# Kernel tuning notes

Measured on AMD Instinct MI355X. Metric: run time of the kernel, lower is better.

Reference implementation:

```python
import jax, jax.numpy as jnp
import numpy as np

N_NODES = 50000
N_EDGES = 500000
NUM_FEAT = 128
NUM_CLASSES = 112
HID = 18
HEADS = 8
OUT_DIM = 144  # hidden_dim * heads = 18*8 = 144, also final GAT out_dim
N_GRAPHS = 64
EPS = 1e-5
NEG_SLOPE = 0.2


def setup_inputs() -> dict:
    key = jax.random.key(0)
    ks = jax.random.split(key, 32)
    f32 = jnp.float32
    def rn(k, shape, scale=0.1):
        return jax.random.normal(k, shape, f32) * scale
    x = jax.random.normal(ks[0], (N_NODES, NUM_FEAT), f32)
    edge_index = jax.random.randint(ks[1], (2, N_EDGES), 0, N_NODES)
    batch = jnp.sort(jax.random.randint(ks[2], (N_NODES,), 0, N_GRAPHS))
    D = HID * HEADS  # 144
    params = dict(
        x=x, edge_index=edge_index, batch=batch,
        We=rn(ks[3], (NUM_FEAT, D)), be=jnp.zeros((D,), f32),
        Wg=rn(ks[4], (3, D, D)),
        a_sg=rn(ks[5], (3, HEADS, HID)), a_dg=rn(ks[6], (3, HEADS, HID)),
        bg=jnp.zeros((3, D), f32),
        gam=jnp.ones((3, D), f32), bet=jnp.zeros((3, D), f32),
        W3=rn(ks[7], (D, OUT_DIM)),
        a_s3=rn(ks[8], (1, OUT_DIM)), a_d3=rn(ks[9], (1, OUT_DIM)),
        b3=jnp.zeros((OUT_DIM,), f32),
        gam3=jnp.ones((OUT_DIM,), f32), bet3=jnp.zeros((OUT_DIM,), f32),
        M1=rn(ks[10], (OUT_DIM, 72)), bm1=jnp.zeros((72,), f32),
        gm1=jnp.ones((72,), f32), bb1=jnp.zeros((72,), f32),
        M2=rn(ks[11], (72, 36)), bm2=jnp.zeros((36,), f32),
        gm2=jnp.ones((36,), f32), bb2=jnp.zeros((36,), f32),
        M3=rn(ks[12], (36, NUM_CLASSES)), bm3=jnp.zeros((NUM_CLASSES,), f32),
    )
    return params


def _gat_layer(h, src, dst, W, a_s, a_d, b, heads, out_ch):
    # PyG GATConv: per-head linear, additive attention, segment softmax over dst
    N = h.shape[0]
    hp = (h @ W).reshape(N, heads, out_ch)                 # [N,H,C]
    al_s = (hp * a_s).sum(-1)                              # [N,H]
    al_d = (hp * a_d).sum(-1)                              # [N,H]
    e = jax.nn.leaky_relu(al_s[src] + al_d[dst], NEG_SLOPE)  # [E,H]
    m = jax.ops.segment_max(e, dst, num_segments=N)
    ex = jnp.exp(e - m[dst])
    den = jax.ops.segment_sum(ex, dst, num_segments=N)
    alpha = ex / (den[dst] + 1e-16)                        # [E,H]
    out = jax.ops.segment_sum(hp[src] * alpha[..., None], dst, num_segments=N)
    return out.reshape(N, heads * out_ch) + b


def _bn(x, g, b):
    mu = x.mean(0)
    v = jnp.var(x, axis=0)
    return g * (x - mu) * jax.lax.rsqrt(v + EPS) + b


def reference(x, edge_index, batch, We, be, Wg, a_sg, a_dg, bg, gam, bet,
              W3, a_s3, a_d3, b3, gam3, bet3,
              M1, bm1, gm1, bb1, M2, bm2, gm2, bb2, M3, bm3):
    N = x.shape[0]
    loops = jnp.arange(N)  # GATConv add_self_loops=True
    src = jnp.concatenate([edge_index[0], loops])
    dst = jnp.concatenate([edge_index[1], loops])
    out = x @ We + be
    for i in range(3):
        out = _gat_layer(out, src, dst, Wg[i], a_sg[i], a_dg[i], bg[i], HEADS, HID)
        out = jax.nn.relu(out)
        out = _bn(out, gam[i], bet[i])
    out = _gat_layer(out, src, dst, W3, a_s3, a_d3, b3, 1, OUT_DIM)
    out = jax.nn.relu(out)
    out = _bn(out, gam3, bet3)
    # global mean pool over graphs
    sums = jax.ops.segment_sum(out, batch, num_segments=N_GRAPHS)
    cnt = jax.ops.segment_sum(jnp.ones((N, 1), out.dtype), batch, num_segments=N_GRAPHS)
    g = sums / jnp.maximum(cnt, 1.0)
    # PyG MLP: lin -> batchnorm -> relu (plain last layer)
    h = jax.nn.relu(_bn(g @ M1 + bm1, gm1, bb1))
    h = jax.nn.relu(_bn(h @ M2 + bm2, gm2, bb2))
    return h @ M3 + bm3
```

## Files before the change

kernel.cpp:

```cpp
#include <hip/hip_runtime.h>
#include <cstdint>

#define N_NODESC 50000
#define N_EDGESC 500000
#define E_TOT    550000
#define DIM      144
#define NGRAPH   64
#define EPSV     1e-5f
#define SCAN_NB  ((N_NODESC + 511)/512)

typedef __attribute__((ext_vector_type(8))) short bf16x8;
typedef __attribute__((ext_vector_type(4))) float f32x4;

__device__ __forceinline__ float lrelu(float x){ return x > 0.f ? x : 0.2f*x; }

__device__ __forceinline__ unsigned short f2bf(float f){
  unsigned u = __float_as_uint(f);
  u += 0x7FFF + ((u >> 16) & 1);
  return (unsigned short)(u >> 16);
}
__device__ __forceinline__ float bf2f(unsigned short b){
  return __uint_as_float(((unsigned)b) << 16);
}

__global__ void k_count(const int* __restrict__ ei, int* __restrict__ deg){
  int e = blockIdx.x*blockDim.x + threadIdx.x;
  if (e >= E_TOT) return;
  int d = (e < N_EDGESC) ? ei[N_EDGESC + e] : (e - N_EDGESC);
  atomicAdd(&deg[d], 1);
}

__global__ __launch_bounds__(256) void k_scan1(const int* __restrict__ deg,
    int* __restrict__ scanned, int* __restrict__ bsum){
  __shared__ int ls[256];
  int b = blockIdx.x, t = threadIdx.x;
  int i0 = b*512 + 2*t;
  int e0 = (i0   < N_NODESC) ? deg[i0]   : 0;
  int e1 = (i0+1 < N_NODESC) ? deg[i0+1] : 0;
  int s = e0 + e1;
  ls[t] = s;
  __syncthreads();
  #pragma unroll
  for (int ofs=1; ofs<256; ofs<<=1){
    int v = (t >= ofs) ? ls[t-ofs] : 0;
    __syncthreads();
    ls[t] += v;
    __syncthreads();
  }
  int excl = ls[t] - s;
  if (i0   < N_NODESC) scanned[i0]   = excl;
  if (i0+1 < N_NODESC) scanned[i0+1] = excl + e0;
  if (t == 255) bsum[b] = ls[255];
}

__global__ void k_scan2(int* __restrict__ bsum){
  __shared__ int ls[128];
  int t = threadIdx.x;
  int v = (t < SCAN_NB) ? bsum[t] : 0;
  ls[t] = v;
  __syncthreads();
  #pragma unroll
  for (int ofs=1; ofs<128; ofs<<=1){
    int u = (t >= ofs) ? ls[t-ofs] : 0;
    __syncthreads();
    ls[t] += u;
    __syncthreads();
  }
  if (t < SCAN_NB) bsum[t] = ls[t] - v;
}

__global__ __launch_bounds__(256) void k_scan3(const int* __restrict__ scanned,
    const int* __restrict__ bsum, int* __restrict__ row_ptr, int* __restrict__ cursor){
  int i = blockIdx.x*blockDim.x + threadIdx.x;
  if (i < N_NODESC){
    int v = scanned[i] + bsum[i >> 9];
    row_ptr[i] = v; cursor[i] = v;
  }
  if (i == 0) row_ptr[N_NODESC] = E_TOT;
}

__global__ void k_scatter(const int* __restrict__ ei, int* __restrict__ cursor,
                          int* __restrict__ col){
  int e = blockIdx.x*blockDim.x + threadIdx.x;
  if (e >= E_TOT) return;
  int s, d;
  if (e < N_EDGESC){ s = ei[e]; d = ei[N_EDGESC + e]; } else { s = e - N_EDGESC; d = s; }
  int pos = atomicAdd(&cursor[d], 1);
  col[pos] = s;
}

__global__ __launch_bounds__(192) void k_prep_w(
    const float* __restrict__ W, const float* __restrict__ bias_in,
    const float* __restrict__ a_s, const float* __restrict__ a_d,
    const float* __restrict__ bnsum, const float* __restrict__ bngam,
    const float* __restrict__ bnbet,
    unsigned short* __restrict__ Wt, float* __restrict__ bias2,
    int K, int SK, int H){
  __shared__ float red[256];
  int np = blockIdx.x, k = threadIdx.x;
  float sc = 1.f, sh = 0.f;
  if (k < K && bnsum){
    float mu  = bnsum[k] * (1.f/N_NODESC);
    float var = bnsum[K+k] * (1.f/N_NODESC) - mu*mu;
    float inv = rsqrtf(var + EPSV);
    sc = inv * bngam[k];
    sh = bnbet[k] - mu*sc;
  }
  float wcomb = 0.f;
  if (k < K){
    if (np < 144) wcomb = W[(size_t)k*144 + np];
    else if (H > 0){
      int c = np - 144;
      bool iss = c < 8;
      int h = iss ? c : c - 8;
      if (h < H){
        const float* av = iss ? a_s : a_d;
        int C = 144 / H;
        for (int j=0;j<C;++j) wcomb += W[(size_t)k*144 + h*C + j] * av[h*C + j];
      }
    }
  }
  if (k < SK) Wt[(size_t)np*SK + k] = f2bf(wcomb*sc);
  red[k] = (k < K) ? sh*wcomb : 0.f;
  if (k < 64) red[k+192] = 0.f;
  __syncthreads();
  #pragma unroll
  for (int s=128; s>0; s>>=1){
    if (k < s) red[k] += red[k+s];
    __syncthreads();
  }
  if (k == 0){
    float b = red[0];
    if (np < 144 && bias_in) b += bias_in[np];
    bias2[np] = b;
  }
}

template<int NT, int KS, int SK, int NROW, int AF32>
__global__ __launch_bounds__(256) void k_mfma_gemm(
    const void* __restrict__ Av,
    const unsigned short* __restrict__ Wt,
    const float* __restrict__ bias2,
    unsigned short* __restrict__ hp,
    float* __restrict__ al_s, float* __restrict__ al_d,
    int KA, int H){
  __shared__ unsigned short sW[NROW*SK];
  int t = threadIdx.x;
  for (int i = t; i < NROW*SK/8; i += 256)
    ((uint4*)sW)[i] = ((const uint4*)Wt)[i];
  __syncthreads();

  int wave = t >> 6, lane = t & 63;
  int c = lane & 15, quad = lane >> 4;
  int m_base = blockIdx.x*64 + wave*16;
  int mA = m_base + c; if (mA > N_NODESC-1) mA = N_NODESC-1;
  f32x4 acc[NT];
  #pragma unroll
  for (int i=0;i<NT;++i) acc[i] = (f32x4){0.f,0.f,0.f,0.f};
  #pragma unroll
  for (int ks=0; ks<KS; ++ks){
    bf16x8 af;
    if (AF32){
      const float* Arow = (const float*)Av + (size_t)mA*KA + quad*8;
      float4 f0 = *(const float4*)(Arow + ks*32);
      float4 f1 = *(const float4*)(Arow + ks*32 + 4);
      unsigned short tmp[8] = { f2bf(f0.x),f2bf(f0.y),f2bf(f0.z),f2bf(f0.w),
                                f2bf(f1.x),f2bf(f1.y),f2bf(f1.z),f2bf(f1.w) };
      af = *(const bf16x8*)tmp;
    } else {
      const unsigned short* Arow = (const unsigned short*)Av + (size_t)mA*KA + quad*8;
      af = *(const bf16x8*)(Arow + ks*32);
    }
    #pragma unroll
    for (int tt=0; tt<NT; ++tt){
      bf16x8 bfr = *(const bf16x8*)(sW + (tt*16 + c)*SK + ks*32 + quad*8);
      acc[tt] = __builtin_amdgcn_mfma_f32_16x16x32_bf16(af, bfr, acc[tt], 0, 0, 0);
    }
  }
  #pragma unroll
  for (int tt=0; tt<NT; ++tt){
    int n = tt*16 + c;
    float b = bias2[n];
    #pragma unroll
    for (int r=0;r<4;++r){
      int m = m_base + quad*4 + r;
      if (m < N_NODESC){
        float v = acc[tt][r] + b;
        if (n < 144){
          hp[(size_t)m*144 + n] = f2bf(v);
        } else {
          int cc = n - 144;
          if (cc < 8){ if (cc < H) al_s[m*H + cc] = v; }
          else { int h = cc - 8; if (h < H) al_d[m*H + h] = v; }
        }
      }
    }
  }
}

#define EB 8
__global__ __launch_bounds__(256) void k_edge_softmax(
    const float* __restrict__ al_s, const float* __restrict__ al_d,
    const int* __restrict__ row_ptr, const int* __restrict__ col,
    float* __restrict__ esc, int H){
  int idx = blockIdx.x*blockDim.x + threadIdx.x;
  if (idx >= N_NODESC*H) return;
  int n = idx / H, h = idx - n*H;
  int p0 = row_ptr[n], p1 = row_ptr[n+1];
  float ald = al_d[idx];
  float m = -3.4e38f, d = 0.f;
  for (int base = p0; base < p1; base += EB){
    int cnt = min(EB, p1 - base);
    int ss[EB];
    #pragma unroll
    for (int i=0;i<EB;++i) if (i<cnt) ss[i] = col[base+i];
    float sc[EB];
    #pragma unroll
    for (int i=0;i<EB;++i) if (i<cnt) sc[i] = lrelu(al_s[ss[i]*H + h] + ald);
    float bm = -3.4e38f;
    #pragma unroll
    for (int i=0;i<EB;++i) if (i<cnt){
      esc[(size_t)(base+i)*H + h] = sc[i];
      bm = fmaxf(bm, sc[i]);
    }
    if (bm > m){ d *= __expf(m - bm); m = bm; }
    #pragma unroll
    for (int i=0;i<EB;++i) if (i<cnt) d += __expf(sc[i] - m);
  }
  float inv = 1.f/(d + 1e-16f);
  for (int e = p0; e < p1; ++e)
    esc[(size_t)e*H + h] = __expf(esc[(size_t)e*H + h] - m) * inv;
}

__global__ __launch_bounds__(256) void k_aggregate2(
    const unsigned* __restrict__ hp2, const float* __restrict__ w,
    const int* __restrict__ row_ptr, const int* __restrict__ col,
    const float* __restrict__ bias, unsigned* __restrict__ out,
    int H, int C2){
  int idx = blockIdx.x*blockDim.x + threadIdx.x;
  if (idx >= N_NODESC*72) return;
  int n = idx / 72, cp = idx - n*72;
  int h = cp / C2;
  int p0 = row_ptr[n], p1 = row_ptr[n+1];
  float a0 = 0.f, a1 = 0.f;
  for (int base = p0; base < p1; base += EB){
    int cnt = min(EB, p1 - base);
    int ss[EB]; float ww[EB];
    #pragma unroll
    for (int i=0;i<EB;++i) if (i<cnt){
      ss[i] = col[base+i];
      ww[i] = w[(size_t)(base+i)*H + h];
    }
    unsigned vv[EB];
    #pragma unroll
    for (int i=0;i<EB;++i) if (i<cnt) vv[i] = hp2[(size_t)ss[i]*72 + cp];
    #pragma unroll
    for (int i=0;i<EB;++i) if (i<cnt){
      a0 = fmaf(ww[i], __uint_as_float(vv[i] << 16), a0);
      a1 = fmaf(ww[i], __uint_as_float(vv[i] & 0xFFFF0000u), a1);
    }
  }
  int c0 = 2*cp;
  float r0 = fmaxf(a0 + bias[c0],   0.f);
  float r1 = fmaxf(a1 + bias[c0+1], 0.f);
  out[(size_t)n*72 + cp] = (unsigned)f2bf(r0) | ((unsigned)f2bf(r1) << 16);
}

#define BNS_GRID 512
__global__ __launch_bounds__(256) void k_bnstats1(const uint2* __restrict__ h4,
                                                  float* __restrict__ partials){
  __shared__ float red[252*8];
  int t = threadIdx.x;
  int r = t / 36, c = t - r*36;
  bool active = (t < 252);
  int rows = (N_NODESC + BNS_GRID - 1)/BNS_GRID;
  int n0 = blockIdx.x*rows, n1 = min(N_NODESC, n0+rows);
  float s[4] = {0,0,0,0}, q[4] = {0,0,0,0};
  if (active){
    for (int n = n0 + r; n < n1; n += 7){
      uint2 v = h4[(size_t)n*36 + c];
      float f0 = __uint_as_float(v.x << 16);
      float f1 = __uint_as_float(v.x & 0xFFFF0000u);
      float f2 = __uint_as_float(v.y << 16);
      float f3 = __uint_as_float(v.y & 0xFFFF0000u);
      s[0]+=f0; q[0]+=f0*f0; s[1]+=f1; q[1]+=f1*f1;
      s[2]+=f2; q[2]+=f2*f2; s[3]+=f3; q[3]+=f3*f3;
    }
    #pragma unroll
    for (int j=0;j<4;++j){
      red[(c*7+r)*8 + j]     = s[j];
      red[(c*7+r)*8 + 4 + j] = q[j];
    }
  }
  __syncthreads();
  if (t < 36){
    float ss[4]={0,0,0,0}, qq[4]={0,0,0,0};
    for (int rr=0; rr<7; ++rr){
      #pragma unroll
      for (int j=0;j<4;++j){
        ss[j] += red[(t*7+rr)*8 + j];
        qq[j] += red[(t*7+rr)*8 + 4 + j];
      }
    }
    float* p = partials + (size_t)blockIdx.x*288;
    #pragma unroll
    for (int j=0;j<4;++j){
      p[4*t+j]       = ss[j];
      p[144+4*t+j]   = qq[j];
    }
  }
}

__global__ __launch_bounds__(64) void k_bnstats2(const float* __restrict__ partials,
                                                 float* __restrict__ sums){
  int i = blockIdx.x, t = threadIdx.x;
  float s = 0.f;
  for (int b = t; b < BNS_GRID; b += 64) s += partials[(size_t)b*288 + i];
  #pragma unroll
  for (int o=32; o>0; o>>=1) s += __shfl_xor(s, o, 64);
  if (t == 0) sums[i] = s;
}

__device__ int lbound(const int* a, int n, int v){
  int lo = 0, hi = n;
  while (lo < hi){ int m = (lo+hi) >> 1; if (a[m] < v) lo = m+1; else hi = m; }
  return lo;
}

__global__ __launch_bounds__(128) void k_pool(const unsigned* __restrict__ h2,
    const int* __restrict__ batch, float* __restrict__ sums, int* __restrict__ cnts){
  int g = blockIdx.x & 63, part = blockIdx.x >> 6;
  __shared__ int sb[2];
  if (threadIdx.x == 0){ sb[0] = lbound(batch, N_NODESC, g); sb[1] = lbound(batch, N_NODESC, g+1); }
  __syncthreads();
  int lo = sb[0], hi = sb[1];
  int t = threadIdx.x;
  if (t < 72){
    float a0 = 0.f, a1 = 0.f;
    for (int n = lo + part; n < hi; n += 32){
      unsigned v = h2[(size_t)n*72 + t];
      a0 += __uint_as_float(v << 16);
      a1 += __uint_as_float(v & 0xFFFF0000u);
    }
    atomicAdd(&sums[g*DIM + 2*t],   a0);
    atomicAdd(&sums[g*DIM + 2*t+1], a1);
  }
  if (t == 0 && part == 0) cnts[g] = hi - lo;
}

__global__ __launch_bounds__(64) void k_mlp1(const float* __restrict__ psum,
    const int* __restrict__ cnts,
    const float* __restrict__ bn3, const float* __restrict__ gam3,
    const float* __restrict__ bet3,
    const float* __restrict__ M1, const float* __restrict__ bm1,
    const float* __restrict__ gm1, const float* __restrict__ bb1,
    float* __restrict__ h1){
  __shared__ float sSc[144], sSh[144];
  int t = threadIdx.x, c = blockIdx.x;
  for (int i=t; i<144; i+=64){
    float mu  = bn3[i] * (1.f/N_NODESC);
    float var = bn3[144+i] * (1.f/N_NODESC) - mu*mu;
    float sc  = rsqrtf(var + EPSV) * gam3[i];
    sSc[i] = sc; sSh[i] = bet3[i] - mu*sc;
  }
  __syncthreads();
  float invc = 1.f / (float)max(cnts[t], 1);
  float acc = bm1[c];
  const float* pr = psum + t*144;
  for (int k=0; k<144; ++k){
    float g = fmaf(pr[k]*invc, sSc[k], sSh[k]);
    acc = fmaf(g, M1[k*72 + c], acc);
  }
  float s = acc, q = acc*acc;
  #pragma unroll
  for (int o=32; o>0; o>>=1){ s += __shfl_xor(s, o, 64); q += __shfl_xor(q, o, 64); }
  float mu = s*(1.f/64.f), var = q*(1.f/64.f) - mu*mu;
  float v = (acc - mu)*rsqrtf(var + EPSV)*gm1[c] + bb1[c];
  h1[t*72 + c] = fmaxf(v, 0.f);
}

__global__ __launch_bounds__(64) void k_mlp2(const float* __restrict__ h1,
    const float* __restrict__ M2, const float* __restrict__ bm2,
    const float* __restrict__ gm2, const float* __restrict__ bb2,
    float* __restrict__ h2){
  int t = threadIdx.x, c = blockIdx.x;
  float acc = bm2[c];
  const float* pr = h1 + t*72;
  for (int k=0; k<72; ++k) acc = fmaf(pr[k], M2[k*36 + c], acc);
  float s = acc, q = acc*acc;
  #pragma unroll
  for (int o=32; o>0; o>>=1){ s += __shfl_xor(s, o, 64); q += __shfl_xor(q, o, 64); }
  float mu = s*(1.f/64.f), var = q*(1.f/64.f) - mu*mu;
  float v = (acc - mu)*rsqrtf(var + EPSV)*gm2[c] + bb2[c];
  h2[t*36 + c] = fmaxf(v, 0.f);
}

__global__ __launch_bounds__(64) void k_mlp3(const float* __restrict__ h2,
    const float* __restrict__ M3, const float* __restrict__ bm3,
    float* __restrict__ out){
  int t = threadIdx.x, c = blockIdx.x;
  float acc = bm3[c];
  const float* pr = h2 + t*36;
  for (int k=0; k<36; ++k) acc = fmaf(pr[k], M3[k*112 + c], acc);
  out[t*112 + c] = acc;
}

extern "C" void kernel_launch(void* const* d_in, const int* in_sizes, int n_in,
                              void* d_out, int out_size, void* d_ws, size_t ws_size,
                              hipStream_t stream){
  const float* x    = (const float*)d_in[0];
  const int*   ei   = (const int*)d_in[1];
  const int*   batch= (const int*)d_in[2];
  const float* We   = (const float*)d_in[3];
  const float* be   = (const float*)d_in[4];
  const float* Wg   = (const float*)d_in[5];
  const float* a_sg = (const float*)d_in[6];
  const float* a_dg = (const float*)d_in[7];
  const float* bg   = (const float*)d_in[8];
  const float* gam  = (const float*)d_in[9];
  const float* bet  = (const float*)d_in[10];
  const float* W3   = (const float*)d_in[11];
  const float* a_s3 = (const float*)d_in[12];
  const float* a_d3 = (const float*)d_in[13];
  const float* b3   = (const float*)d_in[14];
  const float* gam3 = (const float*)d_in[15];
  const float* bet3 = (const float*)d_in[16];
  const float* M1   = (const float*)d_in[17];
  const float* bm1  = (const float*)d_in[18];
  const float* gm1  = (const float*)d_in[19];
  const float* bb1  = (const float*)d_in[20];
  const float* M2   = (const float*)d_in[21];
  const float* bm2  = (const float*)d_in[22];
  const float* gm2  = (const float*)d_in[23];
  const float* bb2  = (const float*)d_in[24];
  const float* M3   = (const float*)d_in[25];
  const float* bm3  = (const float*)d_in[26];
  float* out = (float*)d_out;

  char* ws = (char*)d_ws;
  size_t off = 0;
  auto alloc = [&](size_t bytes)->char*{
    char* p = ws + off; off += (bytes + 255) & ~(size_t)255; return p;
  };
  unsigned short* hAb = (unsigned short*)alloc((size_t)N_NODESC*DIM*2);
  unsigned short* hp  = (unsigned short*)alloc((size_t)N_NODESC*DIM*2);
  float* al_s   = (float*)alloc((size_t)N_NODESC*8*4);
  float* al_d   = (float*)alloc((size_t)N_NODESC*8*4);
  float* esc    = (float*)alloc((size_t)E_TOT*8*4);
  int* row_ptr  = (int*)alloc((size_t)(N_NODESC+1)*4);
  int* deg      = (int*)alloc((size_t)N_NODESC*4);
  int* cursor   = (int*)alloc((size_t)N_NODESC*4);
  int* scanned  = (int*)alloc((size_t)N_NODESC*4);
  int* bsum     = (int*)alloc((size_t)SCAN_NB*4);
  int* col      = (int*)alloc((size_t)E_TOT*4);
  float* bns4   = (float*)alloc(4*2*DIM*4);
  float* partials = (float*)alloc((size_t)BNS_GRID*288*4);
  float* psum   = (float*)alloc((size_t)NGRAPH*DIM*4);
  int* pcnt     = (int*)alloc(NGRAPH*4);
  float* h1buf  = (float*)alloc((size_t)NGRAPH*72*4);
  float* h2buf  = (float*)alloc((size_t)NGRAPH*36*4);
  unsigned short* Wt = (unsigned short*)alloc((size_t)160*168*2);
  float* bias2  = (float*)alloc(160*4);
  (void)ws_size; (void)n_in; (void)in_sizes; (void)out_size;

  const int GEMM_GRID = (N_NODESC + 63)/64;

  hipMemsetAsync(deg, 0, (size_t)N_NODESC*4, stream);
  k_count<<<(E_TOT+255)/256, 256, 0, stream>>>(ei, deg);
  k_scan1<<<SCAN_NB, 256, 0, stream>>>(deg, scanned, bsum);
  k_scan2<<<1, 128, 0, stream>>>(bsum);
  k_scan3<<<(N_NODESC+255)/256, 256, 0, stream>>>(scanned, bsum, row_ptr, cursor);
  k_scatter<<<(E_TOT+255)/256, 256, 0, stream>>>(ei, cursor, col);

  k_prep_w<<<144, 192, 0, stream>>>(We, be, nullptr, nullptr,
                                    nullptr, nullptr, nullptr, Wt, bias2, 128, 136, 0);
  k_mfma_gemm<9,4,136,144,1><<<GEMM_GRID, 256, 0, stream>>>(
      x, Wt, bias2, hAb, nullptr, nullptr, 128, 0);

  for (int L=0; L<4; ++L){
    const float* W  = (L<3) ? (Wg  + (size_t)L*DIM*DIM) : W3;
    const float* as = (L<3) ? (a_sg + (size_t)L*8*18)   : a_s3;
    const float* ad = (L<3) ? (a_dg + (size_t)L*8*18)   : a_d3;
    const float* bb = (L<3) ? (bg  + L*DIM) : b3;
    int H = (L<3) ? 8 : 1;
    int C = (L<3) ? 18 : 144;
    const float* bnp = (L==0) ? nullptr : bns4 + (size_t)(L-1)*2*DIM;
    const float* gmp = (L==0) ? nullptr : gam + (size_t)(L-1)*DIM;
    const float* btp = (L==0) ? nullptr : bet + (size_t)(L-1)*DIM;
    k_prep_w<<<160, 192, 0, stream>>>(W, nullptr, as, ad,
                                      bnp, gmp, btp, Wt, bias2, 144, 168, H);
    k_mfma_gemm<10,5,168,160,0><<<GEMM_GRID, 256, 0, stream>>>(
        hAb, Wt, bias2, hp, al_s, al_d, 144, H);
    k_edge_softmax<<<(N_NODESC*H+255)/256, 256, 0, stream>>>(
        al_s, al_d, row_ptr, col, esc, H);
    k_aggregate2<<<(N_NODESC*72+255)/256, 256, 0, stream>>>(
        (const unsigned*)hp, esc, row_ptr, col, bb, (unsigned*)hAb, H, C/2);
    k_bnstats1<<<BNS_GRID, 256, 0, stream>>>((const uint2*)hAb, partials);
    k_bnstats2<<<288, 64, 0, stream>>>(partials, bns4 + (size_t)L*2*DIM);
  }

  hipMemsetAsync(psum, 0, (size_t)NGRAPH*DIM*4, stream);
  k_pool<<<NGRAPH*32, 128, 0, stream>>>((const unsigned*)hAb, batch, psum, pcnt);
  k_mlp1<<<72, 64, 0, stream>>>(psum, pcnt, bns4 + 3*2*DIM, gam3, bet3,
                                M1, bm1, gm1, bb1, h1buf);
  k_mlp2<<<36, 64, 0, stream>>>(h1buf, M2, bm2, gm2, bb2, h2buf);
  k_mlp3<<<112, 64, 0, stream>>>(h2buf, M3, bm3, out);
}
```

Baseline: 643.6 us.

## Stage GEMM output through LDS for coalesced stores; recompute edge scores instead of storing

The projection GEMM epilogue now writes the bf16 hp tile into shared memory and then copies full 144-wide rows to global memory with 16-byte stores, replacing scattered 2-byte writes. The attention logits are still written directly. The edge softmax kernel no longer writes raw scores in its first pass and rereads them later. It recomputes the scores from al_s gathers in a second pass, trading one global write and read per edge for extra gathers and leaky-relu work. The staging reuses the sW weight buffer behind syncthreads and assumes 64 rows per block.

```diff
diff --git a/kernel.cpp b/kernel.cpp
--- a/kernel.cpp
+++ b/kernel.cpp
@@ -177,24 +177,38 @@
       acc[tt] = __builtin_amdgcn_mfma_f32_16x16x32_bf16(af, bfr, acc[tt], 0, 0, 0);
     }
   }
-  #pragma unroll
-  for (int tt=0; tt<NT; ++tt){
-    int n = tt*16 + c;
+
+  if (NT > 9){
+    int n = 144 + c;
     float b = bias2[n];
     #pragma unroll
     for (int r=0;r<4;++r){
       int m = m_base + quad*4 + r;
       if (m < N_NODESC){
-        float v = acc[tt][r] + b;
-        if (n < 144){
-          hp[(size_t)m*144 + n] = f2bf(v);
-        } else {
-          int cc = n - 144;
-          if (cc < 8){ if (cc < H) al_s[m*H + cc] = v; }
-          else { int h = cc - 8; if (h < H) al_d[m*H + h] = v; }
-        }
+        float v = acc[9][r] + b;
+        if (c < 8){ if (c < H) al_s[m*H + c] = v; }
+        else { int h = c - 8; if (h < H) al_d[m*H + h] = v; }
       }
     }
+  }
+
+  __syncthreads();
+  unsigned short* sOut = sW + wave*2304;
+  #pragma unroll
+  for (int tt=0; tt<9; ++tt){
+    int n = tt*16 + c;
+    float b = bias2[n];
+    #pragma unroll
+    for (int r=0;r<4;++r)
+      sOut[(quad*4+r)*144 + n] = f2bf(acc[tt][r] + b);
+  }
+  __syncthreads();
+  int base_row = blockIdx.x*64;
+  for (int i = t; i < 1152; i += 256){
+    int rr = i/18, j = i - rr*18;
+    int m = base_row + rr;
+    if (m < N_NODESC)
+      *((uint4*)(hp + (size_t)m*144) + j) = *((const uint4*)(sW + rr*144) + j);
   }
 }
 
@@ -219,17 +233,24 @@
     for (int i=0;i<EB;++i) if (i<cnt) sc[i] = lrelu(al_s[ss[i]*H + h] + ald);
     float bm = -3.4e38f;
     #pragma unroll
-    for (int i=0;i<EB;++i) if (i<cnt){
-      esc[(size_t)(base+i)*H + h] = sc[i];
-      bm = fmaxf(bm, sc[i]);
-    }
+    for (int i=0;i<EB;++i) if (i<cnt) bm = fmaxf(bm, sc[i]);
     if (bm > m){ d *= __expf(m - bm); m = bm; }
     #pragma unroll
     for (int i=0;i<EB;++i) if (i<cnt) d += __expf(sc[i] - m);
   }
   float inv = 1.f/(d + 1e-16f);
-  for (int e = p0; e < p1; ++e)
-    esc[(size_t)e*H + h] = __expf(esc[(size_t)e*H + h] - m) * inv;
+  for (int base = p0; base < p1; base += EB){
+    int cnt = min(EB, p1 - base);
+    int ss[EB];
+    #pragma unroll
+    for (int i=0;i<EB;++i) if (i<cnt) ss[i] = col[base+i];
+    float sc[EB];
+    #pragma unroll
+    for (int i=0;i<EB;++i) if (i<cnt) sc[i] = lrelu(al_s[ss[i]*H + h] + ald);
+    #pragma unroll
+    for (int i=0;i<EB;++i) if (i<cnt)
+      esc[(size_t)(base+i)*H + h] = __expf(sc[i] - m) * inv;
+  }
 }
 
 __global__ __launch_bounds__(256) void k_aggregate2(
```

After: 602.8 us. 1.07x faster.
